# Kernel tuning notes

Measured on AMD Instinct MI355X. Metric: run time of the kernel, lower is better.

The kernel has to match this reference:

```python
import jax, jax.numpy as jnp
import numpy as np

H, DH, M, ITERS = 8, 64, 256, 6   # heads, dim_head, num_landmarks, pinv iters
DIM = H * DH                      # 512
KERNEL = 33                       # residual depthwise conv kernel


def setup_inputs() -> dict:
    key = jax.random.key(0)
    ks = jax.random.split(key, 5)
    b, n = 2, 8192                # n multiple of M -> no divisibility padding
    x = jax.random.normal(ks[0], (b, n, DIM), jnp.float32)
    ln_gamma = jnp.ones((DIM,), jnp.float32)
    ln_beta = jnp.zeros((DIM,), jnp.float32)
    w_qkv = jax.random.normal(ks[1], (DIM, 3 * DIM), jnp.float32) * 0.02
    w_out = jax.random.normal(ks[2], (DIM, DIM), jnp.float32) * 0.02
    b_out = jnp.zeros((DIM,), jnp.float32)
    res_kernel = jax.random.normal(ks[3], (H, 1, KERNEL, 1), jnp.float32) * 0.02
    return {"x": x, "ln_gamma": ln_gamma, "ln_beta": ln_beta, "w_qkv": w_qkv,
            "w_out": w_out, "b_out": b_out, "res_kernel": res_kernel}


def _pinv(a, iters):
    # lucidrains moore_penrose_iter_pinv (Newton-Schulz iteration)
    abs_a = jnp.abs(a)
    scale = abs_a.sum(-1).max() * abs_a.sum(-2).max()
    z = jnp.swapaxes(a, -1, -2) / scale
    I = jnp.eye(a.shape[-1], dtype=a.dtype)
    for _ in range(iters):
        az = a @ z
        z = 0.25 * z @ (13.0 * I - az @ (15.0 * I - az @ (7.0 * I - az)))
    return z


def reference(x, ln_gamma, ln_beta, w_qkv, w_out, b_out, res_kernel):
    b, n, d = x.shape
    # pre-LayerNorm (eps 1e-5)
    mu = jnp.mean(x, -1, keepdims=True)
    var = jnp.var(x, -1, keepdims=True)
    xn = (x - mu) * jax.lax.rsqrt(var + 1e-5) * ln_gamma + ln_beta
    # qkv projection (bias-free)
    q, k, v = jnp.split(xn @ w_qkv, 3, axis=-1)
    to_heads = lambda t: t.reshape(b, n, H, DH).transpose(0, 2, 1, 3)  # b h n d
    q, k, v = to_heads(q), to_heads(k), to_heads(v)
    q = q * (DH ** -0.5)
    # landmarks: mean over groups of l consecutive tokens ('(m l) d -> m d')
    l = n // M
    q_l = q.reshape(b, H, M, l, DH).mean(3)  # b h M d
    k_l = k.reshape(b, H, M, l, DH).mean(3)
    sim1 = jnp.einsum('bhnd,bhmd->bhnm', q, k_l)      # queries vs k-landmarks
    sim2 = jnp.einsum('bhid,bhjd->bhij', q_l, k_l)    # landmarks vs landmarks
    sim3 = jnp.einsum('bhmd,bhnd->bhmn', q_l, k)      # q-landmarks vs keys
    a1 = jax.nn.softmax(sim1, axis=-1)
    a2 = jax.nn.softmax(sim2, axis=-1)
    a3 = jax.nn.softmax(sim3, axis=-1)
    a2_inv = _pinv(a2, ITERS)
    out = (a1 @ a2_inv) @ (a3 @ v)  # b h n d
    # residual depthwise conv over the sequence axis (Conv2d kernel (33,1), groups=H)
    pad = KERNEL // 2
    out = out + jax.lax.conv_general_dilated(
        v, res_kernel, (1, 1), [(pad, pad), (0, 0)],
        dimension_numbers=('NCHW', 'OIHW', 'NCHW'), feature_group_count=H)
    out = out.transpose(0, 2, 1, 3).reshape(b, n, d)
    out = out @ w_out + b_out  # to_out Linear (dropout inactive at eval)
    return x + out             # TransLayer residual
```

## Files before the change

### kernel.cpp

```cpp
#include <hip/hip_runtime.h>
#include <math.h>

#define H_ 8
#define DH_ 64
#define DIM_ 512
#define M_ 256
#define N_ 8192
#define BH_ 16
#define LG_ 32
#define KC_ 33
#define CH_ 16
#define NTI_ 8

typedef __attribute__((ext_vector_type(8))) short bf16x8;
typedef __attribute__((ext_vector_type(4))) short s16x4;
typedef __attribute__((ext_vector_type(4))) float f32x4;

__device__ __forceinline__ short f2bf(float f) {
  unsigned u = __float_as_uint(f);
  unsigned r = (u + 0x7FFF + ((u >> 16) & 1)) >> 16;
  return (short)r;
}
__device__ __forceinline__ float bf2f(short s) {
  return __uint_as_float(((unsigned)(unsigned short)s) << 16);
}

__device__ __forceinline__ void mfma_nt_core(const short* __restrict__ A,
                                             const short* __restrict__ Bt, int K,
                                             int m0, int n0, size_t lda, size_t ldb,
                                             f32x4 acc[4][4], short* As, short* Bs) {
  const int tid = threadIdx.x;
  const int wave = tid >> 6, lane = tid & 63;
  const int wr = (wave >> 1) * 64, wc = (wave & 1) * 64;
  const int mi = lane & 15, quad = lane >> 4;
  for (int k0 = 0; k0 < K; k0 += 32) {
#pragma unroll
    for (int t = 0; t < 2; ++t) {
      const int cbase = (t * 4 + wave) * 64;
      const int chunk = cbase + lane;
      const int row = chunk >> 2, cc = (chunk & 3) * 8;
      __builtin_amdgcn_global_load_lds(
          (const __attribute__((address_space(1))) void*)(A + (size_t)(m0 + row) * lda + k0 + cc),
          (__attribute__((address_space(3))) void*)(As + (size_t)cbase * 8), 16, 0, 0);
      __builtin_amdgcn_global_load_lds(
          (const __attribute__((address_space(1))) void*)(Bt + (size_t)(n0 + row) * ldb + k0 + cc),
          (__attribute__((address_space(3))) void*)(Bs + (size_t)cbase * 8), 16, 0, 0);
    }
    __syncthreads();
    bf16x8 af[4], bf[4];
#pragma unroll
    for (int i = 0; i < 4; ++i)
      af[i] = *(const bf16x8*)&As[(wr + i * 16 + mi) * 32 + quad * 8];
#pragma unroll
    for (int j = 0; j < 4; ++j)
      bf[j] = *(const bf16x8*)&Bs[(wc + j * 16 + mi) * 32 + quad * 8];
#pragma unroll
    for (int i = 0; i < 4; ++i)
#pragma unroll
      for (int j = 0; j < 4; ++j)
        acc[i][j] = __builtin_amdgcn_mfma_f32_16x16x32_bf16(af[i], bf[j], acc[i][j], 0, 0, 0);
    __syncthreads();
  }
}

__global__ __launch_bounds__(256) void qkv_mfma(const short* __restrict__ xnb,
                                                const short* __restrict__ wt,
                                                short* __restrict__ qb, short* __restrict__ kb,
                                                short* __restrict__ vb) {
  __shared__ short As[128 * 32], Bs[128 * 32];
  f32x4 acc[4][4] = {};
  const int m0 = blockIdx.x * 128, n0 = blockIdx.y * 128;
  mfma_nt_core(xnb, wt, DIM_, m0, n0, DIM_, DIM_, acc, As, Bs);
  const int wave = threadIdx.x >> 6, lane = threadIdx.x & 63;
  const int wr = (wave >> 1) * 64, wc = (wave & 1) * 64;
  const int mi = lane & 15, quad = lane >> 4;
  const int which = n0 >> 9;
  short* dst = which == 0 ? qb : which == 1 ? kb : vb;
  const float sc = which == 0 ? 0.125f : 1.0f;
#pragma unroll
  for (int j = 0; j < 4; ++j) {
    const int col = n0 + wc + j * 16 + mi;
    const int h = (col >> 6) & 7, d = col & 63;
#pragma unroll
    for (int i = 0; i < 4; ++i) {
#pragma unroll
      for (int r = 0; r < 4; ++r) {
        const int row = m0 + wr + i * 16 + quad * 4 + r;
        const int b = row >> 13, t = row & (N_ - 1);
        dst[((size_t)(b * H_ + h) * N_ + t) * DH_ + d] = f2bf(acc[i][j][r] * sc);
      }
    }
  }
}

__global__ __launch_bounds__(256) void final_mfma(const short* __restrict__ omb,
                                                  const short* __restrict__ wt,
                                                  const float* __restrict__ x,
                                                  const float* __restrict__ bout,
                                                  float* __restrict__ y) {
  __shared__ short As[128 * 32], Bs[128 * 32];
  f32x4 acc[4][4] = {};
  const int m0 = blockIdx.x * 128, n0 = blockIdx.y * 128;
  mfma_nt_core(omb, wt, DIM_, m0, n0, DIM_, DIM_, acc, As, Bs);
  const int wave = threadIdx.x >> 6, lane = threadIdx.x & 63;
  const int wr = (wave >> 1) * 64, wc = (wave & 1) * 64;
  const int mi = lane & 15, quad = lane >> 4;
#pragma unroll
  for (int j = 0; j < 4; ++j) {
    const int col = n0 + wc + j * 16 + mi;
    const float bo = bout[col];
#pragma unroll
    for (int i = 0; i < 4; ++i) {
#pragma unroll
      for (int r = 0; r < 4; ++r) {
        const int row = m0 + wr + i * 16 + quad * 4 + r;
        y[(size_t)row * DIM_ + col] = acc[i][j][r] + x[(size_t)row * DIM_ + col] + bo;
      }
    }
  }
}

__global__ __launch_bounds__(256) void convt_kernel(const float* __restrict__ in,
                                                    short* __restrict__ out, int K, int N) {
  __shared__ float tile[32][33];
  const int n0 = blockIdx.x * 32, k0 = blockIdx.y * 32;
  const int tx = threadIdx.x & 31, ty = threadIdx.x >> 5;
  for (int r = ty; r < 32; r += 8) tile[r][tx] = in[(size_t)(k0 + r) * N + n0 + tx];
  __syncthreads();
  for (int r = ty; r < 32; r += 8) out[(size_t)(n0 + r) * K + k0 + tx] = f2bf(tile[tx][r]);
}

__global__ __launch_bounds__(256) void vt_kernel(const short* __restrict__ vb,
                                                 short* __restrict__ vtb) {
  __shared__ short tile[32][33];
  const int t0 = blockIdx.x * 32, d0 = blockIdx.y * 32, bh = blockIdx.z;
  const int tx = threadIdx.x & 31, ty = threadIdx.x >> 5;
  for (int r = ty; r < 32; r += 8)
    tile[r][tx] = vb[((size_t)bh * N_ + t0 + r) * DH_ + d0 + tx];
  __syncthreads();
  for (int r = ty; r < 32; r += 8)
    vtb[((size_t)bh * DH_ + d0 + r) * N_ + t0 + tx] = tile[tx][r];
}

__global__ __launch_bounds__(128) void ln_kernel(const float* __restrict__ x,
                                                 const float* __restrict__ gamma,
                                                 const float* __restrict__ beta,
                                                 short* __restrict__ xnb) {
  const int row = blockIdx.x, tid = threadIdx.x;
  const float4 v = ((const float4*)(x + (size_t)row * DIM_))[tid];
  float s = v.x + v.y + v.z + v.w;
  float ss = v.x * v.x + v.y * v.y + v.z * v.z + v.w * v.w;
  __shared__ float r1[128], r2[128];
  r1[tid] = s;
  r2[tid] = ss;
  __syncthreads();
  for (int off = 64; off > 0; off >>= 1) {
    if (tid < off) {
      r1[tid] += r1[tid + off];
      r2[tid] += r2[tid + off];
    }
    __syncthreads();
  }
  const float mu = r1[0] * (1.0f / DIM_);
  const float var = r2[0] * (1.0f / DIM_) - mu * mu;
  const float rs = rsqrtf(var + 1e-5f);
  const float4 g = ((const float4*)gamma)[tid];
  const float4 bb = ((const float4*)beta)[tid];
  s16x4 o = {f2bf((v.x - mu) * rs * g.x + bb.x), f2bf((v.y - mu) * rs * g.y + bb.y),
             f2bf((v.z - mu) * rs * g.z + bb.z), f2bf((v.w - mu) * rs * g.w + bb.w)};
  ((s16x4*)(xnb + (size_t)row * DIM_))[tid] = o;
}

__global__ __launch_bounds__(256) void landmark_kernel(const short* __restrict__ qb,
                                                       const short* __restrict__ kb,
                                                       float* __restrict__ ql,
                                                       float* __restrict__ kl,
                                                       short* __restrict__ qlb,
                                                       short* __restrict__ klb) {
  const int idx = blockIdx.x * 256 + threadIdx.x;
  const int d = idx & (DH_ - 1);
  const int m = (idx >> 6) & (M_ - 1);
  const int bh = idx >> 14;
  const size_t base = ((size_t)bh * N_ + m * LG_) * DH_ + d;
  float sq = 0.f, sk = 0.f;
#pragma unroll 8
  for (int t = 0; t < LG_; ++t) {
    sq += bf2f(qb[base + (size_t)t * DH_]);
    sk += bf2f(kb[base + (size_t)t * DH_]);
  }
  sq *= (1.0f / LG_);
  sk *= (1.0f / LG_);
  ql[idx] = sq;
  kl[idx] = sk;
  qlb[idx] = f2bf(sq);
  klb[idx] = f2bf(sk);
}

__global__ __launch_bounds__(256) void sim2_softmax(const float* __restrict__ ql,
                                                    const float* __restrict__ kl,
                                                    float* __restrict__ a2,
                                                    short* __restrict__ a2b) {
  const int i = blockIdx.x, bh = blockIdx.y, j = threadIdx.x;
  __shared__ float qrow[DH_];
  if (j < DH_) qrow[j] = ql[((size_t)bh * M_ + i) * DH_ + j];
  __syncthreads();
  const float* kr = kl + ((size_t)bh * M_ + j) * DH_;
  float s = 0.f;
#pragma unroll 16
  for (int d = 0; d < DH_; ++d) s += qrow[d] * kr[d];
  __shared__ float red[256];
  red[j] = s;
  __syncthreads();
  for (int off = 128; off > 0; off >>= 1) {
    if (j < off) red[j] = fmaxf(red[j], red[j + off]);
    __syncthreads();
  }
  const float mx = red[0];
  __syncthreads();
  const float e = expf(s - mx);
  red[j] = e;
  __syncthreads();
  for (int off = 128; off > 0; off >>= 1) {
    if (j < off) red[j] += red[j + off];
    __syncthreads();
  }
  const float out = e / red[0];
  a2[((size_t)bh * M_ + i) * M_ + j] = out;
  a2b[((size_t)bh * M_ + i) * M_ + j] = f2bf(out);
}

__global__ __launch_bounds__(256) void colmax_kernel(const float* __restrict__ a2,
                                                     unsigned int* __restrict__ scalebits) {
  const int bh = blockIdx.x, j = threadIdx.x;
  const float* mat = a2 + (size_t)bh * M_ * M_;
  float s = 0.f;
  for (int i = 0; i < M_; ++i) s += fabsf(mat[i * M_ + j]);
  __shared__ float red[256];
  red[j] = s;
  __syncthreads();
  for (int off = 128; off > 0; off >>= 1) {
    if (j < off) red[j] = fmaxf(red[j], red[j + off]);
    __syncthreads();
  }
  if (j == 0) atomicMax(scalebits, __float_as_uint(red[0]));
}

__global__ __launch_bounds__(256) void transpose_scale(const float* __restrict__ a2,
                                                       short* __restrict__ z0b,
                                                       const unsigned int* __restrict__ scalebits) {
  const float inv = 1.0f / __uint_as_float(*scalebits);
  const int idx = blockIdx.x * 256 + threadIdx.x;
  const int j = idx & (M_ - 1), i = (idx >> 8) & (M_ - 1), bh = idx >> 16;
  z0b[idx] = f2bf(a2[((size_t)bh * M_ + j) * M_ + i] * inv);
}

__device__ __forceinline__ void ns_core(const short* __restrict__ A, const short* __restrict__ B,
                                        int m0, int n0, short* Bs, f32x4 acc[4]) {
  const int tid = threadIdx.x, wave = tid >> 6, lane = tid & 63;
  const int mi = lane & 15, quad = lane >> 4;
  const int bkk = tid & 31, g = tid >> 5;
  bf16x8 bv[8];
#pragma unroll
  for (int kc = 0; kc < 8; ++kc)
    bv[kc] = *(const bf16x8*)(B + (size_t)(kc * 32 + bkk) * M_ + n0 + g * 8);
  const short* arow = A + (size_t)(m0 + wave * 16 + mi) * M_;
  bf16x8 af[8];
#pragma unroll
  for (int k0 = 0; k0 < 8; ++k0)
    af[k0] = *(const bf16x8*)(arow + k0 * 32 + quad * 8);
#pragma unroll
  for (int kc = 0; kc < 8; ++kc)
#pragma unroll
    for (int e = 0; e < 8; ++e)
      Bs[(g * 8 + e) * 260 + kc * 32 + bkk] = bv[kc][e];
  __syncthreads();
#pragma unroll
  for (int k0 = 0; k0 < 8; ++k0) {
#pragma unroll
    for (int j = 0; j < 4; ++j) {
      union { bf16x8 v; s16x4 h[2]; } bfr;
      const short* bp = &Bs[(j * 16 + mi) * 260 + k0 * 32 + quad * 8];
      bfr.h[0] = *(const s16x4*)bp;
      bfr.h[1] = *(const s16x4*)(bp + 4);
      acc[j] = __builtin_amdgcn_mfma_f32_16x16x32_bf16(af[k0], bfr.v, acc[j], 0, 0, 0);
    }
  }
}

__device__ __forceinline__ int ns_remap() {
  const int lin = blockIdx.y * 16 + blockIdx.x;
  return (lin & 7) * (gridDim.y << 1) + (lin >> 3);
}

__global__ __launch_bounds__(256) void ns_gemm0(const short* __restrict__ A,
                                                const short* __restrict__ B,
                                                short* __restrict__ C) {
  __shared__ short Bs[64 * 260];
  const int id = ns_remap();
  const int bx = id & 15, by = id >> 4;
  const int m0 = (bx >> 2) * 64, n0 = (bx & 3) * 64;
  const size_t mo = (size_t)by * (M_ * M_);
  f32x4 acc[4] = {};
  ns_core(A + mo, B + mo, m0, n0, Bs, acc);
  const int wave = threadIdx.x >> 6, lane = threadIdx.x & 63;
  const int mi = lane & 15, quad = lane >> 4;
#pragma unroll
  for (int j = 0; j < 4; ++j)
#pragma unroll
    for (int r = 0; r < 4; ++r) {
      const int row = m0 + wave * 16 + quad * 4 + r, col = n0 + j * 16 + mi;
      C[mo + (size_t)row * M_ + col] = f2bf(acc[j][r]);
    }
}

__global__ __launch_bounds__(256) void ns_stageA(const short* __restrict__ z,
                                                 const short* __restrict__ y,
                                                 short* __restrict__ p1,
                                                 short* __restrict__ y2,
                                                 short* __restrict__ w) {
  __shared__ short Bs[64 * 260];
  const int id = ns_remap();
  const int bx = id & 15, by = id >> 4;
  const int m0 = (bx >> 2) * 64, n0 = (bx & 3) * 64;
  const int sel = by & 1;
  const size_t mo = (size_t)(by >> 1) * (M_ * M_);
  f32x4 acc[4] = {};
  ns_core((sel ? y : z) + mo, y + mo, m0, n0, Bs, acc);
  const int wave = threadIdx.x >> 6, lane = threadIdx.x & 63;
  const int mi = lane & 15, quad = lane >> 4;
#pragma unroll
  for (int j = 0; j < 4; ++j)
#pragma unroll
    for (int r = 0; r < 4; ++r) {
      const int row = m0 + wave * 16 + quad * 4 + r, col = n0 + j * 16 + mi;
      const size_t idx = mo + (size_t)row * M_ + col;
      if (sel) {
        y2[idx] = f2bf(acc[j][r]);
        w[idx] = f2bf(1.75f * bf2f(y[idx]) - 0.25f * acc[j][r]);
      } else {
        p1[idx] = f2bf(acc[j][r]);
      }
    }
}

__global__ __launch_bounds__(256) void ns_stageB(const short* __restrict__ p1,
                                                 const short* __restrict__ y2,
                                                 const short* __restrict__ w,
                                                 const short* __restrict__ z,
                                                 const short* __restrict__ y,
                                                 short* __restrict__ zo,
                                                 short* __restrict__ yo,
                                                 float* __restrict__ zf, int zonly) {
  __shared__ short Bs[64 * 260];
  const int id = ns_remap();
  const int bx = id & 15, by = id >> 4;
  const int m0 = (bx >> 2) * 64, n0 = (bx & 3) * 64;
  const int sel = zonly ? 0 : (by & 1);
  const size_t mo = (size_t)(zonly ? by : (by >> 1)) * (M_ * M_);
  f32x4 acc[4] = {};
  ns_core((sel ? y2 : p1) + mo, w + mo, m0, n0, Bs, acc);
  const int wave = threadIdx.x >> 6, lane = threadIdx.x & 63;
  const int mi = lane & 15, quad = lane >> 4;
#pragma unroll
  for (int j = 0; j < 4; ++j)
#pragma unroll
    for (int r = 0; r < 4; ++r) {
      const int row = m0 + wave * 16 + quad * 4 + r, col = n0 + j * 16 + mi;
      const size_t idx = mo + (size_t)row * M_ + col;
      if (sel) {
        yo[idx] = f2bf(3.25f * bf2f(y[idx]) - 3.75f * bf2f(y2[idx]) + acc[j][r]);
      } else {
        const float v = 3.25f * bf2f(z[idx]) - 3.75f * bf2f(p1[idx]) + acc[j][r];
        zo[idx] = f2bf(v);
        if (zf) zf[idx] = v;
      }
    }
}

__device__ __forceinline__ void mm_step(float (*As)[68], float (*Bs)[68],
                                        int tr, int tc, float acc[4][4]) {
#pragma unroll
  for (int kk = 0; kk < 16; ++kk) {
    const float4 a4 = *(const float4*)&As[kk][tr * 4];
    const float4 b4 = *(const float4*)&Bs[kk][tc * 4];
    const float a[4] = {a4.x, a4.y, a4.z, a4.w};
    const float b[4] = {b4.x, b4.y, b4.z, b4.w};
#pragma unroll
    for (int i = 0; i < 4; ++i)
#pragma unroll
      for (int j = 0; j < 4; ++j) acc[i][j] = fmaf(a[i], b[j], acc[i][j]);
  }
}

__device__ __forceinline__ void load_a_tile(const float* A, int lda, int m0, int k0,
                                            int tid, float (*As)[68]) {
  const int r = tid >> 2, kq = tid & 3;
  const float4 a4 = *(const float4*)(A + (size_t)(m0 + r) * lda + k0 + kq * 4);
  As[kq * 4 + 0][r] = a4.x;
  As[kq * 4 + 1][r] = a4.y;
  As[kq * 4 + 2][r] = a4.z;
  As[kq * 4 + 3][r] = a4.w;
}

__device__ __forceinline__ void load_b_nn(const float* B, int ldb, int k0, int n0,
                                          int tid, float (*Bs)[68]) {
  const int kr = tid >> 4, c4 = tid & 15;
  const float4 b4 = *(const float4*)(B + (size_t)(k0 + kr) * ldb + n0 + c4 * 4);
  *(float4*)&Bs[kr][c4 * 4] = b4;
}

__global__ __launch_bounds__(256) void gemm_nn64(const float* __restrict__ A, int lda,
                                                 long long strideA,
                                                 const float* __restrict__ B, long long strideB,
                                                 float* __restrict__ C, long long strideC,
                                                 int kchunk) {
  const int bz = blockIdx.z;
  A += (size_t)bz * strideA;
  B += (size_t)bz * strideB;
  C += (size_t)bz * strideC;
  const int m0 = blockIdx.x * 64;
  const int tid = threadIdx.x, tr = tid >> 4, tc = tid & 15;
  __shared__ float As[16][68], Bs[16][68];
  float acc[4][4] = {};
  for (int k0 = 0; k0 < kchunk; k0 += 16) {
    load_a_tile(A, lda, m0, k0, tid, As);
    load_b_nn(B, DH_, k0, 0, tid, Bs);
    __syncthreads();
    mm_step(As, Bs, tr, tc, acc);
    __syncthreads();
  }
#pragma unroll
  for (int i = 0; i < 4; ++i) {
    const int row = m0 + tr * 4 + i;
    *(float4*)(C + (size_t)row * DH_ + tc * 4) =
        make_float4(acc[i][0], acc[i][1], acc[i][2], acc[i][3]);
  }
}

__device__ __forceinline__ void stage_ks(const short* __restrict__ kb, int bh, int n0,
                                         int wave, int lane, short* ks) {
#pragma unroll
  for (int i = 0; i < 2; ++i) {
    const int cb = i * 256 + wave * 64;
    const int c = cb + lane;
    const int row = c >> 3, cc = c & 7;
    __builtin_amdgcn_global_load_lds(
        (const __attribute__((address_space(1))) void*)(
            kb + ((size_t)bh * N_ + n0 + row) * DH_ + ((cc ^ (row & 7)) * 8)),
        (__attribute__((address_space(3))) void*)(ks + (size_t)cb * 8), 16, 0, 0);
  }
}

__device__ __forceinline__ void stage_vs(const short* __restrict__ vtb, int bh, int n0,
                                         int wave, int lane, short* vs) {
#pragma unroll
  for (int i = 0; i < 2; ++i) {
    const int cb = i * 256 + wave * 64;
    const int c = cb + lane;
    const int row = c >> 3, cc = c & 7;
    __builtin_amdgcn_global_load_lds(
        (const __attribute__((address_space(1))) void*)(
            vtb + ((size_t)bh * DH_ + row) * N_ + n0 + ((cc ^ (row & 7)) * 8)),
        (__attribute__((address_space(3))) void*)(vs + (size_t)cb * 8), 16, 0, 0);
  }
}

__global__ __launch_bounds__(256) void a3_flash(const short* __restrict__ qlb,
                                                const short* __restrict__ kb,
                                                const short* __restrict__ vtb,
                                                float* __restrict__ Opart,
                                                float* __restrict__ mpart,
                                                float* __restrict__ lpart) {
  const int chunk = blockIdx.x, rt = blockIdx.y, bh = blockIdx.z;
  __shared__ short ks[2][64 * 64];
  __shared__ short vs[2][64 * 64];
  __shared__ short ps[64 * 64];
  const int tid = threadIdx.x, wave = tid >> 6, lane = tid & 63;
  const int mi = lane & 15, quad = lane >> 4;
  const short* qrow = qlb + ((size_t)bh * M_ + rt * 64 + wave * 16 + mi) * DH_;
  const bf16x8 aq0 = *(const bf16x8*)(qrow + quad * 8);
  const bf16x8 aq1 = *(const bf16x8*)(qrow + 32 + quad * 8);
  float m[4] = {-INFINITY, -INFINITY, -INFINITY, -INFINITY};
  float l[4] = {0.f, 0.f, 0.f, 0.f};
  f32x4 o[4] = {};
  const int nbase = chunk * (N_ / CH_);
  stage_ks(kb, bh, nbase, wave, lane, ks[0]);
  stage_vs(vtb, bh, nbase, wave, lane, vs[0]);
  __syncthreads();
  for (int t = 0; t < NTI_; ++t) {
    const int cur = t & 1;
    if (t + 1 < NTI_) {
      stage_ks(kb, bh, nbase + (t + 1) * 64, wave, lane, ks[cur ^ 1]);
      stage_vs(vtb, bh, nbase + (t + 1) * 64, wave, lane, vs[cur ^ 1]);
    }
    f32x4 s[4];
#pragma unroll
    for (int j = 0; j < 4; ++j) {
      const int row = j * 16 + mi;
      const bf16x8 b0 = *(const bf16x8*)&ks[cur][row * 64 + ((quad ^ (row & 7)) * 8)];
      const bf16x8 b1 = *(const bf16x8*)&ks[cur][row * 64 + (((quad + 4) ^ (row & 7)) * 8)];
      f32x4 z = {0.f, 0.f, 0.f, 0.f};
      z = __builtin_amdgcn_mfma_f32_16x16x32_bf16(aq0, b0, z, 0, 0, 0);
      s[j] = __builtin_amdgcn_mfma_f32_16x16x32_bf16(aq1, b1, z, 0, 0, 0);
    }
    float alpha[4];
#pragma unroll
    for (int r = 0; r < 4; ++r) {
      float v = fmaxf(fmaxf(s[0][r], s[1][r]), fmaxf(s[2][r], s[3][r]));
      v = fmaxf(v, __shfl_xor(v, 1, 64));
      v = fmaxf(v, __shfl_xor(v, 2, 64));
      v = fmaxf(v, __shfl_xor(v, 4, 64));
      v = fmaxf(v, __shfl_xor(v, 8, 64));
      const float mnew = fmaxf(m[r], v);
      alpha[r] = __expf(m[r] - mnew);
      m[r] = mnew;
    }
    float rs[4] = {0.f, 0.f, 0.f, 0.f};
#pragma unroll
    for (int j = 0; j < 4; ++j)
#pragma unroll
      for (int r = 0; r < 4; ++r) {
        const float p = __expf(s[j][r] - m[r]);
        rs[r] += p;
        const int prow = wave * 16 + quad * 4 + r;
        const int pcol = j * 16 + mi;
        ps[prow * 64 + (((pcol >> 3) ^ (prow & 7)) * 8) + (pcol & 7)] = f2bf(p);
      }
#pragma unroll
    for (int r = 0; r < 4; ++r) {
      l[r] = l[r] * alpha[r] + rs[r];
#pragma unroll
      for (int j = 0; j < 4; ++j) o[j][r] *= alpha[r];
    }
    const int prow = wave * 16 + mi;
    const bf16x8 ap0 = *(const bf16x8*)&ps[prow * 64 + ((quad ^ (mi & 7)) * 8)];
    const bf16x8 ap1 = *(const bf16x8*)&ps[prow * 64 + (((quad + 4) ^ (mi & 7)) * 8)];
#pragma unroll
    for (int j = 0; j < 4; ++j) {
      const int vrow = j * 16 + mi;
      const bf16x8 b0 = *(const bf16x8*)&vs[cur][vrow * 64 + ((quad ^ (vrow & 7)) * 8)];
      const bf16x8 b1 = *(const bf16x8*)&vs[cur][vrow * 64 + (((quad + 4) ^ (vrow & 7)) * 8)];
      o[j] = __builtin_amdgcn_mfma_f32_16x16x32_bf16(ap0, b0, o[j], 0, 0, 0);
      o[j] = __builtin_amdgcn_mfma_f32_16x16x32_bf16(ap1, b1, o[j], 0, 0, 0);
    }
    __syncthreads();
  }
#pragma unroll
  for (int r = 0; r < 4; ++r) {
    float v = l[r];
    v += __shfl_xor(v, 1, 64);
    v += __shfl_xor(v, 2, 64);
    v += __shfl_xor(v, 4, 64);
    v += __shfl_xor(v, 8, 64);
    l[r] = v;
  }
  const int p2 = bh * 4 + rt;
  float* Ob = Opart + ((size_t)chunk * 64 + p2) * 4096;
#pragma unroll
  for (int j = 0; j < 4; ++j)
#pragma unroll
    for (int r = 0; r < 4; ++r)
      Ob[(wave * 16 + quad * 4 + r) * 64 + j * 16 + mi] = o[j][r];
  if (mi == 0) {
#pragma unroll
    for (int r = 0; r < 4; ++r) {
      mpart[((size_t)chunk * 64 + p2) * 64 + wave * 16 + quad * 4 + r] = m[r];
      lpart[((size_t)chunk * 64 + p2) * 64 + wave * 16 + quad * 4 + r] = l[r];
    }
  }
}

__global__ __launch_bounds__(256) void a3_combine(const float* __restrict__ Opart,
                                                  const float* __restrict__ mpart,
                                                  const float* __restrict__ lpart,
                                                  float* __restrict__ a3v) {
  const int p2 = blockIdx.x, ds = blockIdx.y;
  const int bh = p2 >> 2, rt = p2 & 3;
  __shared__ float wgt[CH_][64];
  const int tid = threadIdx.x;
  if (tid < 64) {
    float mg = -INFINITY;
#pragma unroll
    for (int c = 0; c < CH_; ++c) mg = fmaxf(mg, mpart[((size_t)c * 64 + p2) * 64 + tid]);
    float e[CH_], lg = 0.f;
#pragma unroll
    for (int c = 0; c < CH_; ++c) {
      e[c] = __expf(mpart[((size_t)c * 64 + p2) * 64 + tid] - mg);
      lg += lpart[((size_t)c * 64 + p2) * 64 + tid] * e[c];
    }
    const float inv = 1.f / lg;
#pragma unroll
    for (int c = 0; c < CH_; ++c) wgt[c][tid] = e[c] * inv;
  }
  __syncthreads();
  for (int i = ds * 1024 + tid; i < ds * 1024 + 1024; i += 256) {
    const int row = i >> 6, d = i & 63;
    float s = 0.f;
#pragma unroll
    for (int c = 0; c < CH_; ++c) s += Opart[((size_t)c * 64 + p2) * 4096 + i] * wgt[c][row];
    a3v[((size_t)bh * M_ + rt * 64 + row) * DH_ + d] = s;
  }
}

__global__ __launch_bounds__(256) void w2t_kernel(const float* __restrict__ w2,
                                                  short* __restrict__ w2tb) {
  const int bh = blockIdx.x, tid = threadIdx.x;
  for (int i = tid; i < M_ * DH_; i += 256) {
    const int r = i >> 6, d = i & 63;
    w2tb[((size_t)bh * DH_ + d) * M_ + r] = f2bf(w2[(size_t)bh * M_ * DH_ + i]);
  }
}

__global__ __launch_bounds__(256, 4) void a1_conv(const short* __restrict__ qb,
                                                  const short* __restrict__ klb,
                                                  const short* __restrict__ w2tb,
                                                  const short* __restrict__ vtb,
                                                  const float* __restrict__ rk,
                                                  short* __restrict__ omb) {
  __shared__ __align__(16) char smem[34944];
  short* kls = (short*)smem;
  short* ps = (short*)smem;
  short* vwin = (short*)(smem + 17920);
  short* band = (short*)(smem + 32768);
  const int bh = blockIdx.y, t0 = blockIdx.x * 64;
  const int b = bh >> 3, h = bh & 7;
  const int tid = threadIdx.x, wave = tid >> 6, lane = tid & 63;
  const int mi = lane & 15, quad = lane >> 4;

  const short* qrow = qb + ((size_t)bh * N_ + t0 + wave * 16 + mi) * DH_;
  const bf16x8 aq0 = *(const bf16x8*)(qrow + quad * 8);
  const bf16x8 aq1 = *(const bf16x8*)(qrow + 32 + quad * 8);

  const int vd = tid & 63, cg0 = tid >> 6;
  bf16x8 vreg[4];
  {
    const short* vrow = vtb + ((size_t)bh * DH_ + vd) * N_;
#pragma unroll
    for (int slot = 0; slot < 4; ++slot) {
      const int ch = cg0 + slot * 4;
      bf16x8 vv = {};
      if (ch < 14) {
        const int tbase = t0 - 16 + ch * 8;
        if (tbase >= 0 && tbase + 8 <= N_) {
          vv = *(const bf16x8*)(vrow + tbase);
        } else {
#pragma unroll
          for (int e = 0; e < 8; ++e) {
            const int tt = tbase + e;
            vv[e] = (tt >= 0 && tt < N_) ? vrow[tt] : (short)0;
          }
        }
      }
      vreg[slot] = vv;
    }
  }
#pragma unroll
  for (int i = 0; i < 4; ++i) {
    const int idx = tid + i * 256;
    const int r = idx >> 6, c = idx & 63, u = c - r;
    band[r * 68 + c] = (u >= 0 && u < KC_) ? f2bf(rk[h * KC_ + u]) : (short)0;
  }

#pragma unroll
  for (int i = 0; i < 8; ++i) {
    const int cb = i * 256 + wave * 64;
    const int c = cb + lane;
    const int row = c >> 3, cc = c & 7;
    __builtin_amdgcn_global_load_lds(
        (const __attribute__((address_space(1))) void*)(
            klb + ((size_t)bh * M_ + row) * DH_ + (cc ^ (row & 7)) * 8),
        (__attribute__((address_space(3))) void*)(kls + (size_t)cb * 8), 16, 0, 0);
  }
  __syncthreads();

  f32x4 s[16] = {};
#pragma unroll
  for (int f = 0; f < 16; ++f) {
    const int row = f * 16 + mi;
    const bf16x8 blo = *(const bf16x8*)&kls[row * 64 + ((quad ^ (row & 7)) * 8)];
    const bf16x8 bhi = *(const bf16x8*)&kls[row * 64 + (((quad + 4) ^ (row & 7)) * 8)];
    f32x4 z = __builtin_amdgcn_mfma_f32_16x16x32_bf16(aq0, blo, s[f], 0, 0, 0);
    s[f] = __builtin_amdgcn_mfma_f32_16x16x32_bf16(aq1, bhi, z, 0, 0, 0);
  }
  float lsum[4];
#pragma unroll
  for (int r = 0; r < 4; ++r) {
    float v = s[0][r];
#pragma unroll
    for (int f = 1; f < 16; ++f) v = fmaxf(v, s[f][r]);
    v = fmaxf(v, __shfl_xor(v, 1, 64));
    v = fmaxf(v, __shfl_xor(v, 2, 64));
    v = fmaxf(v, __shfl_xor(v, 4, 64));
    v = fmaxf(v, __shfl_xor(v, 8, 64));
    float sum = 0.f;
#pragma unroll
    for (int f = 0; f < 16; ++f) {
      const float p = __expf(s[f][r] - v);
      s[f][r] = p;
      sum += p;
    }
    lsum[r] = sum;
  }
  __syncthreads();

#pragma unroll
  for (int slot = 0; slot < 4; ++slot) {
    const int ch = cg0 + slot * 4;
    if (ch < 14) *(bf16x8*)&vwin[vd * 116 + ch * 8] = vreg[slot];
  }

  f32x4 o[4] = {};
#pragma unroll
  for (int half = 0; half < 2; ++half) {
#pragma unroll
    for (int f = 0; f < 8; ++f)
#pragma unroll
      for (int r = 0; r < 4; ++r)
        ps[(wave * 16 + quad * 4 + r) * 140 + f * 16 + mi] = f2bf(s[half * 8 + f][r]);
#pragma unroll
    for (int k0 = 0; k0 < 4; ++k0) {
      union { bf16x8 v; s16x4 hh[2]; } ap;
      const short* pp = &ps[(wave * 16 + mi) * 140 + k0 * 32 + quad * 8];
      ap.hh[0] = *(const s16x4*)pp;
      ap.hh[1] = *(const s16x4*)(pp + 4);
#pragma unroll
      for (int j = 0; j < 4; ++j) {
        const bf16x8 bw = *(const bf16x8*)(w2tb + ((size_t)bh * DH_ + j * 16 + mi) * M_ +
                                           (half * 4 + k0) * 32 + quad * 8);
        o[j] = __builtin_amdgcn_mfma_f32_16x16x32_bf16(ap.v, bw, o[j], 0, 0, 0);
      }
    }
  }
#pragma unroll
  for (int r = 0; r < 4; ++r) {
    float v = lsum[r];
    v += __shfl_xor(v, 1, 64);
    v += __shfl_xor(v, 2, 64);
    v += __shfl_xor(v, 4, 64);
    v += __shfl_xor(v, 8, 64);
    const float inv = 1.f / v;
#pragma unroll
    for (int j = 0; j < 4; ++j) o[j][r] *= inv;
  }
  __syncthreads();

#pragma unroll
  for (int ks = 0; ks < 2; ++ks) {
    union { bf16x8 v; s16x4 hh[2]; } ab;
    const short* bp = &band[mi * 68 + ks * 32 + quad * 8];
    ab.hh[0] = *(const s16x4*)bp;
    ab.hh[1] = *(const s16x4*)(bp + 4);
#pragma unroll
    for (int j = 0; j < 4; ++j) {
      union { bf16x8 v; s16x4 hh[2]; } bv;
      const short* vp = &vwin[(j * 16 + mi) * 116 + wave * 16 + ks * 32 + quad * 8];
      bv.hh[0] = *(const s16x4*)vp;
      bv.hh[1] = *(const s16x4*)(vp + 4);
      o[j] = __builtin_amdgcn_mfma_f32_16x16x32_bf16(ab.v, bv.v, o[j], 0, 0, 0);
    }
  }
#pragma unroll
  for (int j = 0; j < 4; ++j) {
    const int d = j * 16 + mi;
#pragma unroll
    for (int r = 0; r < 4; ++r) {
      const int t = t0 + wave * 16 + quad * 4 + r;
      omb[((size_t)(b * N_ + t)) * DIM_ + h * DH_ + d] = f2bf(o[j][r]);
    }
  }
}

extern "C" void kernel_launch(void* const* d_in, const int* in_sizes, int n_in,
                              void* d_out, int out_size, void* d_ws, size_t ws_size,
                              hipStream_t stream) {
  (void)in_sizes; (void)n_in; (void)out_size;
  const float* x = (const float*)d_in[0];
  const float* gamma = (const float*)d_in[1];
  const float* beta = (const float*)d_in[2];
  const float* wqkv = (const float*)d_in[3];
  const float* wout = (const float*)d_in[4];
  const float* bout = (const float*)d_in[5];
  const float* rk = (const float*)d_in[6];
  float* y = (float*)d_out;
  float* ws = (float*)d_ws;

  size_t o = 0;
  short* xnb = (short*)(ws + o);   o += (size_t)2 * N_ * DIM_ / 2;
  short* wqkvt = (short*)(ws + o); o += (size_t)3 * DIM_ * DIM_ / 2;
  short* woutt = (short*)(ws + o); o += (size_t)DIM_ * DIM_ / 2;
  short* qb = (short*)(ws + o);    o += (size_t)BH_ * N_ * DH_ / 2;
  short* kb = (short*)(ws + o);    o += (size_t)BH_ * N_ * DH_ / 2;
  short* vb = (short*)(ws + o);    o += (size_t)BH_ * N_ * DH_ / 2;
  short* vtb = (short*)(ws + o);   o += (size_t)BH_ * N_ * DH_ / 2;
  float* ql = ws + o;  o += (size_t)BH_ * M_ * DH_;
  float* kl = ws + o;  o += (size_t)BH_ * M_ * DH_;
  short* qlb = (short*)(ws + o); o += (size_t)BH_ * M_ * DH_ / 2;
  short* klb = (short*)(ws + o); o += (size_t)BH_ * M_ * DH_ / 2;
  float* a2 = ws + o;  o += (size_t)BH_ * M_ * M_;
  float* z0f = ws + o; o += (size_t)BH_ * M_ * M_;
  short* a2b = (short*)(ws + o); o += (size_t)BH_ * M_ * M_ / 2;
  short* zb0 = (short*)(ws + o); o += (size_t)BH_ * M_ * M_ / 2;
  short* zb1 = (short*)(ws + o); o += (size_t)BH_ * M_ * M_ / 2;
  short* yb0 = (short*)(ws + o); o += (size_t)BH_ * M_ * M_ / 2;
  short* yb1 = (short*)(ws + o); o += (size_t)BH_ * M_ * M_ / 2;
  short* p1b = (short*)(ws + o); o += (size_t)BH_ * M_ * M_ / 2;
  short* y2b = (short*)(ws + o); o += (size_t)BH_ * M_ * M_ / 2;
  short* wb  = (short*)(ws + o); o += (size_t)BH_ * M_ * M_ / 2;
  float* Opart = ws + o; o += (size_t)CH_ * 64 * 4096;
  float* mpart = ws + o; o += (size_t)CH_ * 64 * 64;
  float* lpart = ws + o; o += (size_t)CH_ * 64 * 64;
  float* a3v = ws + o; o += (size_t)BH_ * M_ * DH_;
  float* w2 = ws + o;  o += (size_t)BH_ * M_ * DH_;
  short* w2tb = (short*)(ws + o); o += (size_t)BH_ * M_ * DH_ / 2;
  short* omb = (short*)(ws + o);  o += (size_t)2 * N_ * DIM_ / 2;
  unsigned int* scalebits = (unsigned int*)(ws + o); o += 16;
  if (ws_size < o * sizeof(float)) return;

  (void)hipMemsetAsync(scalebits, 0, 64, stream);
  ln_kernel<<<2 * N_, 128, 0, stream>>>(x, gamma, beta, xnb);
  convt_kernel<<<dim3(3 * DIM_ / 32, DIM_ / 32), 256, 0, stream>>>(wqkv, wqkvt, DIM_, 3 * DIM_);
  convt_kernel<<<dim3(DIM_ / 32, DIM_ / 32), 256, 0, stream>>>(wout, woutt, DIM_, DIM_);
  qkv_mfma<<<dim3(2 * N_ / 128, 3 * DIM_ / 128), 256, 0, stream>>>(xnb, wqkvt, qb, kb, vb);
  vt_kernel<<<dim3(N_ / 32, 2, BH_), 256, 0, stream>>>(vb, vtb);

  landmark_kernel<<<BH_ * M_ * DH_ / 256, 256, 0, stream>>>(qb, kb, ql, kl, qlb, klb);
  sim2_softmax<<<dim3(M_, BH_), 256, 0, stream>>>(ql, kl, a2, a2b);
  colmax_kernel<<<BH_, 256, 0, stream>>>(a2, scalebits);
  transpose_scale<<<BH_ * M_ * M_ / 256, 256, 0, stream>>>(a2, zb0, scalebits);

  a3_flash<<<dim3(CH_, 4, BH_), 256, 0, stream>>>(qlb, kb, vtb, Opart, mpart, lpart);
  a3_combine<<<dim3(64, 4), 256, 0, stream>>>(Opart, mpart, lpart, a3v);

  ns_gemm0<<<dim3(16, BH_), 256, 0, stream>>>(a2b, zb0, yb0);
  short* zc = zb0; short* zn = zb1; short* yc = yb0; short* yn = yb1;
  for (int it = 0; it < 6; ++it) {
    const int last = (it == 5);
    ns_stageA<<<dim3(16, 2 * BH_), 256, 0, stream>>>(zc, yc, p1b, y2b, wb);
    ns_stageB<<<dim3(16, last ? BH_ : 2 * BH_), 256, 0, stream>>>(
        p1b, y2b, wb, zc, yc, zn, yn, last ? z0f : nullptr, last);
    short* t;
    t = zc; zc = zn; zn = t;
    t = yc; yc = yn; yn = t;
  }

  gemm_nn64<<<dim3(M_ / 64, 1, BH_), 256, 0, stream>>>(
      z0f, M_, (long long)M_ * M_, a3v, (long long)M_ * DH_, w2, (long long)M_ * DH_, M_);
  w2t_kernel<<<BH_, 256, 0, stream>>>(w2, w2tb);

  a1_conv<<<dim3(N_ / 64, BH_), 256, 0, stream>>>(qb, klb, w2tb, vtb, rk, omb);

  final_mfma<<<dim3(2 * N_ / 128, DIM_ / 128), 256, 0, stream>>>(omb, woutt, x, bout, y);
}
```

Measured before the change: 445.1 us.

## Process two token tiles per a1_conv block with prefetch; warp-per-row LayerNorm

The a1_conv kernel now handles two 64-token tiles per block. The landmark-key tile in LDS is loaded once and reused across both tiles, and Q rows and the V window for the next tile are prefetched into registers while the current tile is computed. The P staging buffer is split into 64-column chunks so it can share LDS with the V window. LayerNorm is rewritten to use one wavefront per row with shuffle reductions and 8-wide stores, replacing the shared-memory tree reduction. The trade-offs are larger LDS use and more registers, which may lower occupancy, plus half as many a1_conv blocks.

```diff
diff --git a/kernel.cpp b/kernel.cpp
--- a/kernel.cpp
+++ b/kernel.cpp
@@ -11,6 +11,7 @@
 #define KC_ 33
 #define CH_ 16
 #define NTI_ 8
+#define A1T_ 2
 
 typedef __attribute__((ext_vector_type(8))) short bf16x8;
 typedef __attribute__((ext_vector_type(4))) short s16x4;
@@ -142,33 +143,37 @@
     vtb[((size_t)bh * DH_ + d0 + r) * N_ + t0 + tx] = tile[tx][r];
 }
 
-__global__ __launch_bounds__(128) void ln_kernel(const float* __restrict__ x,
+__global__ __launch_bounds__(256) void ln_kernel(const float* __restrict__ x,
                                                  const float* __restrict__ gamma,
                                                  const float* __restrict__ beta,
                                                  short* __restrict__ xnb) {
-  const int row = blockIdx.x, tid = threadIdx.x;
-  const float4 v = ((const float4*)(x + (size_t)row * DIM_))[tid];
-  float s = v.x + v.y + v.z + v.w;
-  float ss = v.x * v.x + v.y * v.y + v.z * v.z + v.w * v.w;
-  __shared__ float r1[128], r2[128];
-  r1[tid] = s;
-  r2[tid] = ss;
-  __syncthreads();
-  for (int off = 64; off > 0; off >>= 1) {
-    if (tid < off) {
-      r1[tid] += r1[tid + off];
-      r2[tid] += r2[tid + off];
-    }
-    __syncthreads();
-  }
-  const float mu = r1[0] * (1.0f / DIM_);
-  const float var = r2[0] * (1.0f / DIM_) - mu * mu;
+  const int row = blockIdx.x * 4 + (threadIdx.x >> 6);
+  const int lane = threadIdx.x & 63;
+  const float4* xr = (const float4*)(x + (size_t)row * DIM_) + lane * 2;
+  const float4 v0 = xr[0], v1 = xr[1];
+  float s = v0.x + v0.y + v0.z + v0.w + v1.x + v1.y + v1.z + v1.w;
+  float ss = v0.x * v0.x + v0.y * v0.y + v0.z * v0.z + v0.w * v0.w +
+             v1.x * v1.x + v1.y * v1.y + v1.z * v1.z + v1.w * v1.w;
+#pragma unroll
+  for (int off = 1; off < 64; off <<= 1) {
+    s += __shfl_xor(s, off, 64);
+    ss += __shfl_xor(ss, off, 64);
+  }
+  const float mu = s * (1.0f / DIM_);
+  const float var = ss * (1.0f / DIM_) - mu * mu;
   const float rs = rsqrtf(var + 1e-5f);
-  const float4 g = ((const float4*)gamma)[tid];
-  const float4 bb = ((const float4*)beta)[tid];
-  s16x4 o = {f2bf((v.x - mu) * rs * g.x + bb.x), f2bf((v.y - mu) * rs * g.y + bb.y),
-             f2bf((v.z - mu) * rs * g.z + bb.z), f2bf((v.w - mu) * rs * g.w + bb.w)};
-  ((s16x4*)(xnb + (size_t)row * DIM_))[tid] = o;
+  const float4 g0 = ((const float4*)gamma)[lane * 2], g1 = ((const float4*)gamma)[lane * 2 + 1];
+  const float4 b0 = ((const float4*)beta)[lane * 2], b1 = ((const float4*)beta)[lane * 2 + 1];
+  bf16x8 o;
+  o[0] = f2bf((v0.x - mu) * rs * g0.x + b0.x);
+  o[1] = f2bf((v0.y - mu) * rs * g0.y + b0.y);
+  o[2] = f2bf((v0.z - mu) * rs * g0.z + b0.z);
+  o[3] = f2bf((v0.w - mu) * rs * g0.w + b0.w);
+  o[4] = f2bf((v1.x - mu) * rs * g1.x + b1.x);
+  o[5] = f2bf((v1.y - mu) * rs * g1.y + b1.y);
+  o[6] = f2bf((v1.z - mu) * rs * g1.z + b1.z);
+  o[7] = f2bf((v1.w - mu) * rs * g1.w + b1.w);
+  *(bf16x8*)(xnb + (size_t)row * DIM_ + lane * 8) = o;
 }
 
 __global__ __launch_bounds__(256) void landmark_kernel(const short* __restrict__ qb,
@@ -611,55 +616,23 @@
   }
 }
 
-__global__ __launch_bounds__(256, 4) void a1_conv(const short* __restrict__ qb,
-                                                  const short* __restrict__ klb,
-                                                  const short* __restrict__ w2tb,
-                                                  const short* __restrict__ vtb,
-                                                  const float* __restrict__ rk,
-                                                  short* __restrict__ omb) {
-  __shared__ __align__(16) char smem[34944];
+__global__ __launch_bounds__(256) void a1_conv(const short* __restrict__ qb,
+                                               const short* __restrict__ klb,
+                                               const short* __restrict__ w2tb,
+                                               const short* __restrict__ vtb,
+                                               const float* __restrict__ rk,
+                                               short* __restrict__ omb) {
+  __shared__ __align__(16) char smem[49792];
   short* kls = (short*)smem;
-  short* ps = (short*)smem;
-  short* vwin = (short*)(smem + 17920);
-  short* band = (short*)(smem + 32768);
-  const int bh = blockIdx.y, t0 = blockIdx.x * 64;
+  short* work = (short*)(smem + 32768);
+  short* band = (short*)(smem + 47616);
+  short* ps = work;
+  short* vwin = work;
+  const int bh = blockIdx.y, tb = blockIdx.x * (A1T_ * 64);
   const int b = bh >> 3, h = bh & 7;
   const int tid = threadIdx.x, wave = tid >> 6, lane = tid & 63;
   const int mi = lane & 15, quad = lane >> 4;
-
-  const short* qrow = qb + ((size_t)bh * N_ + t0 + wave * 16 + mi) * DH_;
-  const bf16x8 aq0 = *(const bf16x8*)(qrow + quad * 8);
-  const bf16x8 aq1 = *(const bf16x8*)(qrow + 32 + quad * 8);
-
   const int vd = tid & 63, cg0 = tid >> 6;
-  bf16x8 vreg[4];
-  {
-    const short* vrow = vtb + ((size_t)bh * DH_ + vd) * N_;
-#pragma unroll
-    for (int slot = 0; slot < 4; ++slot) {
-      const int ch = cg0 + slot * 4;
-      bf16x8 vv = {};
-      if (ch < 14) {
-        const int tbase = t0 - 16 + ch * 8;
-        if (tbase >= 0 && tbase + 8 <= N_) {
-          vv = *(const bf16x8*)(vrow + tbase);
-        } else {
-#pragma unroll
-          for (int e = 0; e < 8; ++e) {
-            const int tt = tbase + e;
-            vv[e] = (tt >= 0 && tt < N_) ? vrow[tt] : (short)0;
-          }
-        }
-      }
-      vreg[slot] = vv;
-    }
-  }
-#pragma unroll
-  for (int i = 0; i < 4; ++i) {
-    const int idx = tid + i * 256;
-    const int r = idx >> 6, c = idx & 63, u = c - r;
-    band[r * 68 + c] = (u >= 0 && u < KC_) ? f2bf(rk[h * KC_ + u]) : (short)0;
-  }
 
 #pragma unroll
   for (int i = 0; i < 8; ++i) {
@@ -671,101 +644,188 @@
             klb + ((size_t)bh * M_ + row) * DH_ + (cc ^ (row & 7)) * 8),
         (__attribute__((address_space(3))) void*)(kls + (size_t)cb * 8), 16, 0, 0);
   }
-  __syncthreads();
-
-  f32x4 s[16] = {};
-#pragma unroll
-  for (int f = 0; f < 16; ++f) {
-    const int row = f * 16 + mi;
-    const bf16x8 blo = *(const bf16x8*)&kls[row * 64 + ((quad ^ (row & 7)) * 8)];
-    const bf16x8 bhi = *(const bf16x8*)&kls[row * 64 + (((quad + 4) ^ (row & 7)) * 8)];
-    f32x4 z = __builtin_amdgcn_mfma_f32_16x16x32_bf16(aq0, blo, s[f], 0, 0, 0);
-    s[f] = __builtin_amdgcn_mfma_f32_16x16x32_bf16(aq1, bhi, z, 0, 0, 0);
-  }
-  float lsum[4];
-#pragma unroll
-  for (int r = 0; r < 4; ++r) {
-    float v = s[0][r];
-#pragma unroll
-    for (int f = 1; f < 16; ++f) v = fmaxf(v, s[f][r]);
-    v = fmaxf(v, __shfl_xor(v, 1, 64));
-    v = fmaxf(v, __shfl_xor(v, 2, 64));
-    v = fmaxf(v, __shfl_xor(v, 4, 64));
-    v = fmaxf(v, __shfl_xor(v, 8, 64));
-    float sum = 0.f;
+#pragma unroll
+  for (int i = 0; i < 4; ++i) {
+    const int idx = tid + i * 256;
+    const int r = idx >> 6, c = idx & 63, u = c - r;
+    band[r * 68 + c] = (u >= 0 && u < KC_) ? f2bf(rk[h * KC_ + u]) : (short)0;
+  }
+
+  const short* qrow0 = qb + ((size_t)bh * N_ + tb + wave * 16 + mi) * DH_;
+  bf16x8 aqA = *(const bf16x8*)(qrow0 + quad * 8);
+  bf16x8 aqB = *(const bf16x8*)(qrow0 + 32 + quad * 8);
+  bf16x8 vr0, vr1, vr2, vr3;
+  {
+    const short* vrow = vtb + ((size_t)bh * DH_ + vd) * N_;
+#pragma unroll
+    for (int slot = 0; slot < 4; ++slot) {
+      const int ch = cg0 + slot * 4;
+      bf16x8 vv = {};
+      if (ch < 14) {
+        const int tbase = tb - 16 + ch * 8;
+        if (tbase >= 0 && tbase + 8 <= N_) {
+          vv = *(const bf16x8*)(vrow + tbase);
+        } else {
+#pragma unroll
+          for (int e = 0; e < 8; ++e) {
+            const int tt = tbase + e;
+            vv[e] = (tt >= 0 && tt < N_) ? vrow[tt] : (short)0;
+          }
+        }
+      }
+      if (slot == 0) vr0 = vv;
+      else if (slot == 1) vr1 = vv;
+      else if (slot == 2) vr2 = vv;
+      else vr3 = vv;
+    }
+  }
+  __syncthreads();
+
+#pragma unroll
+  for (int tile = 0; tile < A1T_; ++tile) {
+    const int t0 = tb + tile * 64;
+    bf16x8 aqAn = {}, aqBn = {};
+    bf16x8 vn0 = {}, vn1 = {}, vn2 = {}, vn3 = {};
+    if (tile + 1 < A1T_) {
+      const short* qrown = qb + ((size_t)bh * N_ + t0 + 64 + wave * 16 + mi) * DH_;
+      aqAn = *(const bf16x8*)(qrown + quad * 8);
+      aqBn = *(const bf16x8*)(qrown + 32 + quad * 8);
+      const short* vrow = vtb + ((size_t)bh * DH_ + vd) * N_;
+#pragma unroll
+      for (int slot = 0; slot < 4; ++slot) {
+        const int ch = cg0 + slot * 4;
+        bf16x8 vv = {};
+        if (ch < 14) {
+          const int tbase = t0 + 64 - 16 + ch * 8;
+          if (tbase >= 0 && tbase + 8 <= N_) {
+            vv = *(const bf16x8*)(vrow + tbase);
+          } else {
+#pragma unroll
+            for (int e = 0; e < 8; ++e) {
+              const int tt = tbase + e;
+              vv[e] = (tt >= 0 && tt < N_) ? vrow[tt] : (short)0;
+            }
+          }
+        }
+        if (slot == 0) vn0 = vv;
+        else if (slot == 1) vn1 = vv;
+        else if (slot == 2) vn2 = vv;
+        else vn3 = vv;
+      }
+    }
+
+    f32x4 s[16] = {};
 #pragma unroll
     for (int f = 0; f < 16; ++f) {
-      const float p = __expf(s[f][r] - v);
-      s[f][r] = p;
-      sum += p;
-    }
-    lsum[r] = sum;
-  }
-  __syncthreads();
-
-#pragma unroll
-  for (int slot = 0; slot < 4; ++slot) {
-    const int ch = cg0 + slot * 4;
-    if (ch < 14) *(bf16x8*)&vwin[vd * 116 + ch * 8] = vreg[slot];
-  }
-
-  f32x4 o[4] = {};
-#pragma unroll
-  for (int half = 0; half < 2; ++half) {
-#pragma unroll
-    for (int f = 0; f < 8; ++f)
-#pragma unroll
-      for (int r = 0; r < 4; ++r)
-        ps[(wave * 16 + quad * 4 + r) * 140 + f * 16 + mi] = f2bf(s[half * 8 + f][r]);
-#pragma unroll
-    for (int k0 = 0; k0 < 4; ++k0) {
-      union { bf16x8 v; s16x4 hh[2]; } ap;
-      const short* pp = &ps[(wave * 16 + mi) * 140 + k0 * 32 + quad * 8];
-      ap.hh[0] = *(const s16x4*)pp;
-      ap.hh[1] = *(const s16x4*)(pp + 4);
+      const int row = f * 16 + mi;
+      const bf16x8 blo = *(const bf16x8*)&kls[row * 64 + ((quad ^ (row & 7)) * 8)];
+      const bf16x8 bhi = *(const bf16x8*)&kls[row * 64 + (((quad + 4) ^ (row & 7)) * 8)];
+      f32x4 z = __builtin_amdgcn_mfma_f32_16x16x32_bf16(aqA, blo, s[f], 0, 0, 0);
+      s[f] = __builtin_amdgcn_mfma_f32_16x16x32_bf16(aqB, bhi, z, 0, 0, 0);
+    }
+    float lsum[4];
+#pragma unroll
+    for (int r = 0; r < 4; ++r) {
+      float v = s[0][r];
+#pragma unroll
+      for (int f = 1; f < 16; ++f) v = fmaxf(v, s[f][r]);
+      v = fmaxf(v, __shfl_xor(v, 1, 64));
+      v = fmaxf(v, __shfl_xor(v, 2, 64));
+      v = fmaxf(v, __shfl_xor(v, 4, 64));
+      v = fmaxf(v, __shfl_xor(v, 8, 64));
+      float sum = 0.f;
+#pragma unroll
+      for (int f = 0; f < 16; ++f) {
+        const float p = __expf(s[f][r] - v);
+        s[f][r] = p;
+        sum += p;
+      }
+      lsum[r] = sum;
+    }
+    __syncthreads();
+
+    f32x4 o[4] = {};
+#pragma unroll
+    for (int half = 0; half < 2; ++half) {
+#pragma unroll
+      for (int sub = 0; sub < 2; ++sub) {
+#pragma unroll
+        for (int f = 0; f < 4; ++f)
+#pragma unroll
+          for (int r = 0; r < 4; ++r)
+            ps[(wave * 16 + quad * 4 + r) * 76 + f * 16 + mi] =
+                f2bf(s[half * 8 + sub * 4 + f][r]);
+#pragma unroll
+        for (int k0 = 0; k0 < 2; ++k0) {
+          union { bf16x8 v; s16x4 hh[2]; } ap;
+          const short* pp = &ps[(wave * 16 + mi) * 76 + k0 * 32 + quad * 8];
+          ap.hh[0] = *(const s16x4*)pp;
+          ap.hh[1] = *(const s16x4*)(pp + 4);
+#pragma unroll
+          for (int j = 0; j < 4; ++j) {
+            const bf16x8 bw = *(const bf16x8*)(w2tb + ((size_t)bh * DH_ + j * 16 + mi) * M_ +
+                                               half * 128 + sub * 64 + k0 * 32 + quad * 8);
+            o[j] = __builtin_amdgcn_mfma_f32_16x16x32_bf16(ap.v, bw, o[j], 0, 0, 0);
+          }
+        }
+      }
+    }
+#pragma unroll
+    for (int r = 0; r < 4; ++r) {
+      float v = lsum[r];
+      v += __shfl_xor(v, 1, 64);
+      v += __shfl_xor(v, 2, 64);
+      v += __shfl_xor(v, 4, 64);
+      v += __shfl_xor(v, 8, 64);
+      const float inv = 1.f / v;
+#pragma unroll
+      for (int j = 0; j < 4; ++j) o[j][r] *= inv;
+    }
+    __syncthreads();
+
+    {
+#pragma unroll
+      for (int slot = 0; slot < 4; ++slot) {
+        const int ch = cg0 + slot * 4;
+        if (ch < 14) {
+          const bf16x8 vv = slot == 0 ? vr0 : slot == 1 ? vr1 : slot == 2 ? vr2 : vr3;
+          *(bf16x8*)&vwin[vd * 116 + ch * 8] = vv;
+        }
+      }
+    }
+    __syncthreads();
+
+#pragma unroll
+    for (int ks = 0; ks < 2; ++ks) {
+      union { bf16x8 v; s16x4 hh[2]; } ab;
+      const short* bp = &band[mi * 68 + ks * 32 + quad * 8];
+      ab.hh[0] = *(const s16x4*)bp;
+      ab.hh[1] = *(const s16x4*)(bp + 4);
 #pragma unroll
       for (int j = 0; j < 4; ++j) {
-        const bf16x8 bw = *(const bf16x8*)(w2tb + ((size_t)bh * DH_ + j * 16 + mi) * M_ +
-                                           (half * 4 + k0) * 32 + quad * 8);
-        o[j] = __builtin_amdgcn_mfma_f32_16x16x32_bf16(ap.v, bw, o[j], 0, 0, 0);
-      }
-    }
-  }
-#pragma unroll
-  for (int r = 0; r < 4; ++r) {
-    float v = lsum[r];
-    v += __shfl_xor(v, 1, 64);
-    v += __shfl_xor(v, 2, 64);
-    v += __shfl_xor(v, 4, 64);
-    v += __shfl_xor(v, 8, 64);
-    const float inv = 1.f / v;
-#pragma unroll
-    for (int j = 0; j < 4; ++j) o[j][r] *= inv;
-  }
-  __syncthreads();
-
-#pragma unroll
-  for (int ks = 0; ks < 2; ++ks) {
-    union { bf16x8 v; s16x4 hh[2]; } ab;
-    const short* bp = &band[mi * 68 + ks * 32 + quad * 8];
-    ab.hh[0] = *(const s16x4*)bp;
-    ab.hh[1] = *(const s16x4*)(bp + 4);
+        union { bf16x8 v; s16x4 hh[2]; } bv;
+        const short* vp = &vwin[(j * 16 + mi) * 116 + wave * 16 + ks * 32 + quad * 8];
+        bv.hh[0] = *(const s16x4*)vp;
+        bv.hh[1] = *(const s16x4*)(vp + 4);
+        o[j] = __builtin_amdgcn_mfma_f32_16x16x32_bf16(ab.v, bv.v, o[j], 0, 0, 0);
+      }
+    }
 #pragma unroll
     for (int j = 0; j < 4; ++j) {
-      union { bf16x8 v; s16x4 hh[2]; } bv;
-      const short* vp = &vwin[(j * 16 + mi) * 116 + wave * 16 + ks * 32 + quad * 8];
-      bv.hh[0] = *(const s16x4*)vp;
-      bv.hh[1] = *(const s16x4*)(vp + 4);
-      o[j] = __builtin_amdgcn_mfma_f32_16x16x32_bf16(ab.v, bv.v, o[j], 0, 0, 0);
-    }
-  }
-#pragma unroll
-  for (int j = 0; j < 4; ++j) {
-    const int d = j * 16 + mi;
-#pragma unroll
-    for (int r = 0; r < 4; ++r) {
-      const int t = t0 + wave * 16 + quad * 4 + r;
-      omb[((size_t)(b * N_ + t)) * DIM_ + h * DH_ + d] = f2bf(o[j][r]);
+      const int d = j * 16 + mi;
+#pragma unroll
+      for (int r = 0; r < 4; ++r) {
+        const int t = t0 + wave * 16 + quad * 4 + r;
+        omb[((size_t)(b * N_ + t)) * DIM_ + h * DH_ + d] = f2bf(o[j][r]);
+      }
+    }
+    if (tile + 1 < A1T_) {
+      aqA = aqAn;
+      aqB = aqBn;
+      vr0 = vn0;
+      vr1 = vn1;
+      vr2 = vn2;
+      vr3 = vn3;
     }
   }
 }
@@ -817,7 +877,7 @@
   if (ws_size < o * sizeof(float)) return;
 
   (void)hipMemsetAsync(scalebits, 0, 64, stream);
-  ln_kernel<<<2 * N_, 128, 0, stream>>>(x, gamma, beta, xnb);
+  ln_kernel<<<2 * N_ / 4, 256, 0, stream>>>(x, gamma, beta, xnb);
   convt_kernel<<<dim3(3 * DIM_ / 32, DIM_ / 32), 256, 0, stream>>>(wqkv, wqkvt, DIM_, 3 * DIM_);
   convt_kernel<<<dim3(DIM_ / 32, DIM_ / 32), 256, 0, stream>>>(wout, woutt, DIM_, DIM_);
   qkv_mfma<<<dim3(2 * N_ / 128, 3 * DIM_ / 128), 256, 0, stream>>>(xnb, wqkvt, qb, kb, vb);
@@ -847,7 +907,7 @@
       z0f, M_, (long long)M_ * M_, a3v, (long long)M_ * DH_, w2, (long long)M_ * DH_, M_);
   w2t_kernel<<<BH_, 256, 0, stream>>>(w2, w2tb);
 
-  a1_conv<<<dim3(N_ / 64, BH_), 256, 0, stream>>>(qb, klb, w2tb, vtb, rk, omb);
+  a1_conv<<<dim3(N_ / (A1T_ * 64), BH_), 256, 0, stream>>>(qb, klb, w2tb, vtb, rk, omb);
 
   final_mfma<<<dim3(2 * N_ / 128, DIM_ / 128), 256, 0, stream>>>(omb, woutt, x, bout, y);
 }
```

New measurement: 456.4 us. 1.03x slower.
